# Kernel tuning notes

Hardware: AMD Instinct MI355X
Metric: run time of the kernel (lower is better)

Reference implementation:

```python
import math
import jax, jax.numpy as jnp
import numpy as np

# dims (match init_kwargs)
N, K = 10000, 32            # nodes, padded neighbors per node
IN_F, H, HEADS = 128, 128, 8
T_F, R_F, OUT, LAYERS = 64, 32, 64, 2
HD = H // HEADS
START_T, END_T = 0.25, 0.75
ATTN_NORM = math.sqrt(1.0 / HD)
T_NORM = math.sqrt(1.0 / (T_F // 2))
EPS = 1e-5


def layernorm(x, g, b):
    m = jnp.mean(x, axis=-1, keepdims=True)
    v = jnp.var(x, axis=-1, keepdims=True)
    return (x - m) * jax.lax.rsqrt(v + EPS) * g + b


def t2v(dt, Wt, bt):
    # TimeKernel: linear(1->T_F/2) then interleaved [sin, cos] * norm
    h = dt[..., None] * Wt + bt                      # [..., T_F/2]
    return jnp.stack([jnp.sin(h), jnp.cos(h)], axis=-1).reshape(*h.shape[:-1], T_F) * T_NORM


def tgat_layer(x, neighbors, times, rels, mask,
               Wkqv, Wt, bt, Wtime, Wedge, g1, b1n, g2, b2n, W1, bl1, W2, bl2):
    xn = layernorm(x, g1, b1n)
    kqv = xn @ Wkqv                                  # [N, 3H], chunk order (k, q, v)
    k_, q_, v_ = jnp.split(kqv, 3, axis=1)
    kn = k_[neighbors]                               # [N, K, H] irregular gather
    vn = v_[neighbors]
    # per-node time reference: max over [start_t; masked times] (times>=start_t so start_t covered)
    tmax = jnp.max(jnp.where(mask, times, START_T), axis=1)        # [N]
    tq_emb = t2v(tmax - START_T, Wt, bt)             # [N, T_F] (the prepended start_t row)
    tn_emb = t2v(tmax[:, None] - times, Wt, bt)      # [N, K, T_F]
    t_qq = (tq_emb @ Wtime)[:, H:2 * H]              # query chunk of time KQV
    tkn = tn_emb @ Wtime                             # [N, K, 3H]
    re = rels @ Wedge                                # [N, K, 3H]
    q = q_ + t_qq                                    # [N, H]
    k = kn + tkn[..., :H] + re[..., :H]
    v = vn + tkn[..., 2 * H:] + re[..., 2 * H:]
    qh = q.reshape(N, HEADS, HD)
    kh = k.reshape(N, K, HEADS, HD)
    vh = v.reshape(N, K, HEADS, HD)
    scores = jnp.einsum('nhd,nkhd->nhk', qh, kh) * ATTN_NORM
    scores = jnp.where(mask[:, None, :], scores, -1e30)
    attn = jax.nn.softmax(scores, axis=-1)
    out = jnp.einsum('nhk,nkhd->nhd', attn, vh).reshape(N, H)
    has = jnp.any(mask, axis=1)                      # nodes with zero valid neighbors -> zeros
    h = jnp.where(has[:, None], out, 0.0)
    h2 = h + xn
    hn = layernorm(h2, g2, b2n)
    z = jnp.concatenate([xn, hn], axis=1)
    z = jax.nn.relu(z @ W1 + bl1) @ W2 + bl2
    return z + h2


def setup_inputs() -> dict:
    key = jax.random.key(0)
    ks = jax.random.split(key, 16)
    w = lambda i, *shape: jax.random.normal(ks[i], shape, dtype=jnp.float32) * 0.05
    return {
        'x': jax.random.normal(ks[0], (N, IN_F), dtype=jnp.float32),
        'neighbors': jax.random.randint(ks[1], (N, K), 0, N, dtype=jnp.int32),
        'times': jax.random.uniform(ks[2], (N, K), dtype=jnp.float32),
        'rels': jax.random.normal(ks[3], (N, K, R_F), dtype=jnp.float32),
        'Wp': w(4, IN_F, H), 'bp': jnp.zeros((H,), jnp.float32),
        'Wkqv': w(5, H, 3 * H),
        'Wt': w(6, T_F // 2), 'bt': jnp.zeros((T_F // 2,), jnp.float32),
        'Wtime': w(7, T_F, 3 * H),
        'Wedge': w(8, R_F, 3 * H),
        'g1': jnp.ones((H,), jnp.float32), 'b1n': jnp.zeros((H,), jnp.float32),
        'g2': jnp.ones((H,), jnp.float32), 'b2n': jnp.zeros((H,), jnp.float32),
        'W1': w(9, 2 * H, H), 'bl1': jnp.zeros((H,), jnp.float32),
        'W2': w(10, H, H), 'bl2': jnp.zeros((H,), jnp.float32),
        'Wo': w(11, H, OUT), 'bo': jnp.zeros((OUT,), jnp.float32),
    }


def reference(x, neighbors, times, rels, Wp, bp, Wkqv, Wt, bt, Wtime, Wedge,
              g1, b1n, g2, b2n, W1, bl1, W2, bl2, Wo, bo):
    mask = (times >= START_T) & (times < END_T)      # [N, K] temporal neighbor mask
    h = jax.nn.relu(x @ Wp + bp)
    for _ in range(LAYERS):                          # layers SHARE weights (ModuleList([layer]*layers))
        h = tgat_layer(h, neighbors, times, rels, mask,
                       Wkqv, Wt, bt, Wtime, Wedge, g1, b1n, g2, b2n, W1, bl1, W2, bl2)
    return h @ Wo + bo
```

## Files before the change

### kernel.cpp

```cpp
#include <hip/hip_runtime.h>
#include <hip/hip_bf16.h>

#define NN 10000
#define KK 32
#define HH 128
#define TFH 32
#define RFE 32
#define OUTF 64
#define START_T 0.25f
#define END_T 0.75f
#define ATTN_NORM 0.25f
#define T_NORM 0.17677669529663687f
#define LN_EPS 1e-5f
#define MT 64

typedef __attribute__((ext_vector_type(4))) float f32x4;
typedef __attribute__((ext_vector_type(8))) short bf16x8;

__device__ __forceinline__ ushort f2bf(float x){
  __hip_bfloat16 b = __float2bfloat16(x);
  return *(ushort*)&b;
}
__device__ __forceinline__ float bf2f(ushort u){
  __hip_bfloat16 b = *(__hip_bfloat16*)&u;
  return __bfloat162float(b);
}

__device__ __forceinline__ float groupsum32(float v){
  v += __shfl_xor(v, 16, 32);
  v += __shfl_xor(v, 8, 32);
  v += __shfl_xor(v, 4, 32);
  v += __shfl_xor(v, 2, 32);
  v += __shfl_xor(v, 1, 32);
  return v;
}

__device__ __forceinline__ float wavesum64(float v){
  v += __shfl_xor(v, 32, 64);
  v += __shfl_xor(v, 16, 64);
  v += __shfl_xor(v, 8, 64);
  v += __shfl_xor(v, 4, 64);
  v += __shfl_xor(v, 2, 64);
  v += __shfl_xor(v, 1, 64);
  return v;
}

__global__ __launch_bounds__(256) void k_prep_wT(const float* __restrict__ Wp, const float* __restrict__ Wkqv,
    const float* __restrict__ W1, const float* __restrict__ W2, const float* __restrict__ Wo,
    const float* __restrict__ Wtime, const float* __restrict__ Wedge,
    ushort* __restrict__ WpT, ushort* __restrict__ WkqvT, ushort* __restrict__ W1T,
    ushort* __restrict__ W2T, ushort* __restrict__ WoT, ushort* __restrict__ WcT){
  int id = blockIdx.x*256 + threadIdx.x;
  if (id < 16384){ int n=id>>7, k=id&127; WpT[id]=f2bf(Wp[k*HH+n]); return; }
  id -= 16384;
  if (id < 49152){ int n=id>>7, k=id&127; WkqvT[id]=f2bf(Wkqv[k*384+n]); return; }
  id -= 49152;
  if (id < 32768){ int n=id>>8, k=id&255; W1T[id]=f2bf(W1[k*HH+n]); return; }
  id -= 32768;
  if (id < 16384){ int n=id>>7, k=id&127; W2T[id]=f2bf(W2[k*HH+n]); return; }
  id -= 16384;
  if (id < 8192){ int n=id>>7, k=id&127; WoT[id]=f2bf(Wo[k*OUTF+n]); return; }
  id -= 8192;
  if (id < 24576){
    const int c = id/96, r = id%96;
    const int cc = (c < 128) ? c : (c + 128);
    const float v = (r < 64) ? Wtime[r*384 + cc] : Wedge[(r-64)*384 + cc];
    WcT[c*96 + r] = f2bf(v);
  }
}

#define LDA1 136
#define LDA 104
#define LDKV 264

__global__ __launch_bounds__(256) void k_node_proj(
    const float* __restrict__ X, const ushort* __restrict__ WpT, const float* __restrict__ bp,
    float* __restrict__ Y,
    const float* __restrict__ times, const int* __restrict__ nbrs,
    const float* __restrict__ Wt, const float* __restrict__ bt, const float* __restrict__ Wtime,
    float* __restrict__ tqq, float* __restrict__ tmaxb,
    int* __restrict__ cntb, uint* __restrict__ vmaskb, int* __restrict__ nbrC){
  __shared__ ushort As[16*LDA1];
  __shared__ float temb2[2][2*TFH];
  __shared__ float tmax_sh[2];
  const int tid = threadIdx.x;
  if (blockIdx.x < NN/16){
    const int n0 = blockIdx.x*16;
    #pragma unroll
    for (int p=0;p<2;++p){
      const int idx = tid + p*256;
      const int row = idx>>5, c4 = (idx&31)*4;
      const float4 v = *(const float4*)&X[(size_t)(n0+row)*HH + c4];
      *(ushort4*)&As[row*LDA1 + c4] = make_ushort4(f2bf(v.x), f2bf(v.y), f2bf(v.z), f2bf(v.w));
    }
    __syncthreads();
    const int w = tid>>6, lane = tid&63;
    const int lr = lane&15, lk8 = (lane>>4)*8, rbase = (lane>>4)*4;
    bf16x8 a[4];
    #pragma unroll
    for (int kk=0;kk<4;kk++) a[kk] = *(const bf16x8*)&As[lr*LDA1 + kk*32 + lk8];
    f32x4 acc[2];
    #pragma unroll
    for (int nt=0;nt<2;nt++) acc[nt] = (f32x4){0.f,0.f,0.f,0.f};
    #pragma unroll
    for (int nt=0;nt<2;nt++){
      const int n = w*2 + nt;
      #pragma unroll
      for (int kk=0;kk<4;kk++){
        bf16x8 b = *(const bf16x8*)&WpT[(n*16+lr)*HH + kk*32 + lk8];
        acc[nt] = __builtin_amdgcn_mfma_f32_16x16x32_bf16(a[kk], b, acc[nt],0,0,0);
      }
    }
    #pragma unroll
    for (int nt=0;nt<2;nt++){
      const int c = (w*2+nt)*16 + lr;
      const float bj = bp[c];
      #pragma unroll
      for (int r=0;r<4;r++)
        Y[(size_t)(n0 + rbase + r)*HH + c] = fmaxf(acc[nt][r] + bj, 0.f);
    }
  } else {
    const int node0 = (blockIdx.x - NN/16)*2;
    if (tid < MT){
      const int i = tid>>5, k = tid&31;
      const int node = node0 + i;
      const float t = times[node*KK + k];
      const bool valid = (t >= START_T) && (t < END_T);
      float val = valid ? t : START_T;
      #pragma unroll
      for (int off=16; off; off>>=1) val = fmaxf(val, __shfl_xor(val, off, 32));
      const unsigned long long bal = __ballot(valid);
      const uint vm = (uint)(bal >> (i*32));
      if (valid){
        const int slot = __popc(vm & ((1u<<k)-1));
        nbrC[node*KK + slot] = nbrs[node*KK + k];
      }
      if (k==0){ cntb[node] = __popc(vm); vmaskb[node] = vm; tmaxb[node] = val; tmax_sh[i] = val; }
    }
    __syncthreads();
    if (tid < MT){
      const int i = tid>>5, f = tid&31;
      const float hh = fmaf(tmax_sh[i] - START_T, Wt[f], bt[f]);
      temb2[i][2*f]   = __sinf(hh)*T_NORM;
      temb2[i][2*f+1] = __cosf(hh)*T_NORM;
    }
    __syncthreads();
    {
      const int i = tid>>7, jj = tid&127;
      float acc = 0.f;
      #pragma unroll
      for (int f=0; f<2*TFH; f++) acc = fmaf(temb2[i][f], Wtime[f*384 + HH + jj], acc);
      tqq[(size_t)(node0+i)*HH + jj] = acc;
    }
  }
}

__global__ __launch_bounds__(256) void k_kv0_ln0(
    const float* __restrict__ times, const float* __restrict__ rels, const float* __restrict__ tmaxb,
    const float* __restrict__ Wt, const float* __restrict__ bt, const ushort* __restrict__ WcT,
    const uint* __restrict__ vmaskb, uint4* __restrict__ kvout,
    const float* __restrict__ Hin, const ushort* __restrict__ WkqvT,
    const float* __restrict__ g1, const float* __restrict__ b1, const float* __restrict__ tqq,
    float* __restrict__ XN, ushort* __restrict__ xnb,
    float* __restrict__ Qf, ushort* __restrict__ KVb){
  __shared__ ushort smem[MT*LDKV];
  __shared__ float dt_sh[MT];
  const int tid = threadIdx.x;
  if (blockIdx.x < NN/16){
    ushort* As = smem;
    const int n0 = blockIdx.x*16;
    const int grp = tid>>5, gl = tid&31;
    {
      const float4 gv = *(const float4*)&g1[gl*4];
      const float4 bv = *(const float4*)&b1[gl*4];
      #pragma unroll
      for (int rr=0; rr<2; ++rr){
        const int row = grp + rr*8;
        const int node = n0 + row;
        float4 hv = *(const float4*)&Hin[(size_t)node*HH + gl*4];
        float s = hv.x+hv.y+hv.z+hv.w;
        s = groupsum32(s);
        const float mean = s*(1.f/HH);
        const float dx=hv.x-mean, dy=hv.y-mean, dz=hv.z-mean, dw=hv.w-mean;
        float vs = dx*dx+dy*dy+dz*dz+dw*dw;
        vs = groupsum32(vs);
        const float rstd = rsqrtf(vs*(1.f/HH)+LN_EPS);
        const float x0=dx*rstd*gv.x+bv.x, x1=dy*rstd*gv.y+bv.y, x2=dz*rstd*gv.z+bv.z, x3=dw*rstd*gv.w+bv.w;
        ushort4 pk = make_ushort4(f2bf(x0), f2bf(x1), f2bf(x2), f2bf(x3));
        *(ushort4*)&As[row*LDA1 + gl*4] = pk;
        *(float4*)&XN[(size_t)node*HH + gl*4] = make_float4(x0,x1,x2,x3);
        *(ushort4*)&xnb[(size_t)node*HH + gl*4] = pk;
      }
    }
    __syncthreads();
    const int w = tid>>6, lane = tid&63;
    const int lr = lane&15, lk8 = (lane>>4)*8, rbase = (lane>>4)*4;
    bf16x8 a[4];
    #pragma unroll
    for (int kk=0;kk<4;kk++) a[kk] = *(const bf16x8*)&As[lr*LDA1 + kk*32 + lk8];
    f32x4 acc[6];
    #pragma unroll
    for (int nt=0;nt<6;nt++) acc[nt] = (f32x4){0.f,0.f,0.f,0.f};
    #pragma unroll
    for (int nt=0;nt<6;nt++){
      const int n = w*6 + nt;
      #pragma unroll
      for (int kk=0;kk<4;kk++){
        bf16x8 b = *(const bf16x8*)&WkqvT[(n*16+lr)*HH + kk*32 + lk8];
        acc[nt] = __builtin_amdgcn_mfma_f32_16x16x32_bf16(a[kk], b, acc[nt],0,0,0);
      }
    }
    #pragma unroll
    for (int nt=0;nt<6;nt++){
      const int c = (w*6+nt)*16 + lr;
      #pragma unroll
      for (int r=0;r<4;r++){
        const int node = n0 + rbase + r;
        const float v = acc[nt][r];
        if (c < HH)           KVb[(size_t)node*256 + 2*c] = f2bf(v);
        else if (c < 2*HH)    Qf[(size_t)node*HH + (c-HH)] = v + tqq[(size_t)node*HH + (c-HH)];
        else                  KVb[(size_t)node*256 + 2*(c-2*HH) + 1] = f2bf(v);
      }
    }
  } else {
    ushort* Fa = smem;
    ushort* kvs = smem;
    const int node0 = (blockIdx.x - NN/16)*2;
    if (tid < MT){
      const int node = node0 + (tid>>5);
      dt_sh[tid] = tmaxb[node] - times[node*KK + (tid&31)];
    }
    __syncthreads();
    #pragma unroll
    for (int s0=0; s0<8; ++s0){
      const int s = tid + s0*256;
      const int p = s>>5, f = s&31;
      const float hh = fmaf(dt_sh[p], Wt[f], bt[f]);
      ushort2 pk;
      pk.x = f2bf(__sinf(hh)*T_NORM);
      pk.y = f2bf(__cosf(hh)*T_NORM);
      *(ushort2*)&Fa[p*LDA + 2*f] = pk;
    }
    #pragma unroll
    for (int s0=0; s0<2; ++s0){
      const int i = tid + s0*256;
      const int p = i>>3, seg = i&7;
      const float4 rv = *(const float4*)&rels[((size_t)node0*KK + p)*RFE + seg*4];
      ushort4 w2; w2.x=f2bf(rv.x); w2.y=f2bf(rv.y); w2.z=f2bf(rv.z); w2.w=f2bf(rv.w);
      *(ushort4*)&Fa[p*LDA + 64 + seg*4] = w2;
    }
    __syncthreads();
    const int wave = tid>>6, lane = tid&63;
    const int lr = lane&15, lk = (lane>>4)*8;
    f32x4 acc[4][4];
    #pragma unroll
    for (int m=0;m<4;m++)
      #pragma unroll
      for (int n=0;n<4;n++) acc[m][n] = (f32x4){0.f,0.f,0.f,0.f};
    #pragma unroll
    for (int kk=0; kk<3; ++kk){
      const int k0 = kk*32;
      bf16x8 a[4], b[4];
      #pragma unroll
      for (int m=0;m<4;m++) a[m] = *(const bf16x8*)&Fa[(m*16 + lr)*LDA + k0 + lk];
      #pragma unroll
      for (int n=0;n<4;n++) b[n] = *(const bf16x8*)&WcT[(wave*64 + n*16 + lr)*96 + k0 + lk];
      #pragma unroll
      for (int m=0;m<4;m++)
        #pragma unroll
        for (int n=0;n<4;n++)
          acc[m][n] = __builtin_amdgcn_mfma_f32_16x16x32_bf16(a[m], b[n], acc[m][n], 0,0,0);
    }
    __syncthreads();
    const int rbase = (lane>>4)*4;
    #pragma unroll
    for (int n=0;n<4;n++){
      const int c = wave*64 + n*16 + lr;
      const int ip = (c < 128) ? (2*c) : (2*(c-128)+1);
      #pragma unroll
      for (int m=0;m<4;m++)
        #pragma unroll
        for (int r=0;r<4;r++)
          kvs[(m*16 + rbase + r)*LDKV + ip] = f2bf(acc[m][n][r]);
    }
    __syncthreads();
    const uint vm0 = vmaskb[node0], vm1 = vmaskb[node0+1];
    #pragma unroll
    for (int pass=0; pass<8; ++pass){
      const int idx = pass*256 + tid;
      const int row = idx>>5, seg = idx&31;
      const int nloc = row>>5, k = row&31;
      const uint vm = nloc ? vm1 : vm0;
      if ((vm>>k)&1u){
        const int slot = __popc(vm & ((1u<<k)-1));
        const uint4 v = *(const uint4*)&kvs[row*LDKV + seg*8];
        kvout[((size_t)(node0+nloc)*KK + slot)*32 + seg] = v;
      }
    }
  }
}

__global__ __launch_bounds__(256) void k_ln_kqv_mfma(const float* __restrict__ Hin, const ushort* __restrict__ WkqvT,
    const float* __restrict__ g1, const float* __restrict__ b1, const float* __restrict__ tqq,
    float* __restrict__ XN, ushort* __restrict__ xnb,
    float* __restrict__ Qf, ushort* __restrict__ KVb){
  __shared__ ushort As[16*LDA1];
  const int tid = threadIdx.x, n0 = blockIdx.x*16;
  const int grp = tid>>5, gl = tid&31;
  {
    const float4 gv = *(const float4*)&g1[gl*4];
    const float4 bv = *(const float4*)&b1[gl*4];
    #pragma unroll
    for (int rr=0; rr<2; ++rr){
      const int row = grp + rr*8;
      const int node = n0 + row;
      float4 hv = *(const float4*)&Hin[(size_t)node*HH + gl*4];
      float s = hv.x+hv.y+hv.z+hv.w;
      s = groupsum32(s);
      const float mean = s*(1.f/HH);
      const float dx=hv.x-mean, dy=hv.y-mean, dz=hv.z-mean, dw=hv.w-mean;
      float vs = dx*dx+dy*dy+dz*dz+dw*dw;
      vs = groupsum32(vs);
      const float rstd = rsqrtf(vs*(1.f/HH)+LN_EPS);
      const float x0=dx*rstd*gv.x+bv.x, x1=dy*rstd*gv.y+bv.y, x2=dz*rstd*gv.z+bv.z, x3=dw*rstd*gv.w+bv.w;
      ushort4 pk = make_ushort4(f2bf(x0), f2bf(x1), f2bf(x2), f2bf(x3));
      *(ushort4*)&As[row*LDA1 + gl*4] = pk;
      *(float4*)&XN[(size_t)node*HH + gl*4] = make_float4(x0,x1,x2,x3);
      *(ushort4*)&xnb[(size_t)node*HH + gl*4] = pk;
    }
  }
  __syncthreads();
  const int w = tid>>6, lane = tid&63;
  const int lr = lane&15, lk8 = (lane>>4)*8, rbase = (lane>>4)*4;
  bf16x8 a[4];
  #pragma unroll
  for (int kk=0;kk<4;kk++) a[kk] = *(const bf16x8*)&As[lr*LDA1 + kk*32 + lk8];
  f32x4 acc[6];
  #pragma unroll
  for (int nt=0;nt<6;nt++) acc[nt] = (f32x4){0.f,0.f,0.f,0.f};
  #pragma unroll
  for (int nt=0;nt<6;nt++){
    const int n = w*6 + nt;
    #pragma unroll
    for (int kk=0;kk<4;kk++){
      bf16x8 b = *(const bf16x8*)&WkqvT[(n*16+lr)*HH + kk*32 + lk8];
      acc[nt] = __builtin_amdgcn_mfma_f32_16x16x32_bf16(a[kk], b, acc[nt],0,0,0);
    }
  }
  #pragma unroll
  for (int nt=0;nt<6;nt++){
    const int c = (w*6+nt)*16 + lr;
    #pragma unroll
    for (int r=0;r<4;r++){
      const int node = n0 + rbase + r;
      const float v = acc[nt][r];
      if (c < HH)           KVb[(size_t)node*256 + 2*c] = f2bf(v);
      else if (c < 2*HH)    Qf[(size_t)node*HH + (c-HH)] = v + tqq[(size_t)node*HH + (c-HH)];
      else                  KVb[(size_t)node*256 + 2*(c-2*HH) + 1] = f2bf(v);
    }
  }
}

__global__ __launch_bounds__(256) void k_attn6(
    const float* __restrict__ Qf, const uint2* __restrict__ KVu2, const uint2* __restrict__ kvaddC2,
    const int* __restrict__ nbrC, const int* __restrict__ cntb,
    const float* __restrict__ XN, const float* __restrict__ g2, const float* __restrict__ b2,
    float* __restrict__ H2, ushort* __restrict__ hnb){
  __shared__ int nbr_sh[4][KK];
  const int tid = threadIdx.x, node0 = blockIdx.x*4;
  if (tid < 128) nbr_sh[tid>>5][tid&31] = nbrC[(node0 + (tid>>5))*KK + (tid&31)];
  __syncthreads();
  const int wv = tid>>6, l = tid&63;
  const int node = node0 + wv;
  const int cnt = cntb[node];
  const float2 q2 = *(const float2*)&Qf[(size_t)node*HH + 2*l];
  const float q0s = q2.x * ATTN_NORM, q1s = q2.y * ATTN_NORM;
  const uint2* karow = kvaddC2 + (size_t)node*KK*64 + l;
  float m_ = -3.0e38f, sume = 0.f, a0 = 0.f, a1 = 0.f;
  const int cc = (cnt + 7) >> 3;
  for (int ch=0; ch<cc; ++ch){
    const int base = ch*8;
    uint2 ka[8], kb[8];
    #pragma unroll
    for (int i=0;i<8;i++){
      int slot = base + i; slot = (slot < cnt) ? slot : (cnt-1);
      ka[i] = karow[(size_t)slot*64];
      kb[i] = KVu2[(size_t)nbr_sh[wv][slot]*64 + l];
    }
    float s[8];
    #pragma unroll
    for (int i=0;i<8;i++){
      float p = q0s * (bf2f((ushort)(kb[i].x&0xffff)) + bf2f((ushort)(ka[i].x&0xffff)))
              + q1s * (bf2f((ushort)(kb[i].y&0xffff)) + bf2f((ushort)(ka[i].y&0xffff)));
      p += __shfl_xor(p, 4, 8);
      p += __shfl_xor(p, 2, 8);
      p += __shfl_xor(p, 1, 8);
      s[i] = (base + i < cnt) ? p : -1e30f;
    }
    float cm = s[0];
    #pragma unroll
    for (int i=1;i<8;i++) cm = fmaxf(cm, s[i]);
    const float mn = fmaxf(m_, cm);
    const float sc = __expf(m_ - mn);
    sume *= sc; a0 *= sc; a1 *= sc;
    #pragma unroll
    for (int i=0;i<8;i++){
      const float e = __expf(s[i] - mn);
      sume += e;
      a0 = fmaf(e, bf2f((ushort)(kb[i].x>>16)) + bf2f((ushort)(ka[i].x>>16)), a0);
      a1 = fmaf(e, bf2f((ushort)(kb[i].y>>16)) + bf2f((ushort)(ka[i].y>>16)), a1);
    }
    m_ = mn;
  }
  const float inv = (cnt > 0) ? (1.f / sume) : 0.f;
  const float2 xn2 = *(const float2*)&XN[(size_t)node*HH + 2*l];
  const float h0 = a0*inv + xn2.x;
  const float h1 = a1*inv + xn2.y;
  *(float2*)&H2[(size_t)node*HH + 2*l] = make_float2(h0, h1);
  const float mean = wavesum64(h0 + h1) * (1.f/HH);
  const float d0 = h0 - mean, d1 = h1 - mean;
  const float var = wavesum64(d0*d0 + d1*d1) * (1.f/HH);
  const float rstd = rsqrtf(var + LN_EPS);
  const float2 gv = *(const float2*)&g2[2*l];
  const float2 bv = *(const float2*)&b2[2*l];
  ushort2 hn;
  hn.x = f2bf(d0*rstd*gv.x + bv.x);
  hn.y = f2bf(d1*rstd*gv.y + bv.y);
  *(ushort2*)&hnb[(size_t)node*HH + 2*l] = hn;
}

#define LDA2 264
template<int LAST>
__global__ __launch_bounds__(256) void k_ffn_mfma(const ushort* __restrict__ xnb, const ushort* __restrict__ hnb,
    const float* __restrict__ H2, const ushort* __restrict__ W1T, const float* __restrict__ bl1,
    const ushort* __restrict__ W2T, const float* __restrict__ bl2, float* __restrict__ HOUT,
    const ushort* __restrict__ WoT, const float* __restrict__ bo, float* __restrict__ OUT){
  __shared__ ushort As[16*LDA2];
  __shared__ ushort Ms[16*LDA1];
  const int tid = threadIdx.x, n0 = blockIdx.x*16;
  {
    const int row = tid>>4, c8 = (tid&15)*8;
    *(uint4*)&As[row*LDA2 + c8]       = *(const uint4*)&xnb[(size_t)(n0+row)*HH + c8];
    *(uint4*)&As[row*LDA2 + 128 + c8] = *(const uint4*)&hnb[(size_t)(n0+row)*HH + c8];
  }
  __syncthreads();
  const int w = tid>>6, lane = tid&63;
  const int lr = lane&15, lk8 = (lane>>4)*8, rbase = (lane>>4)*4;
  {
    bf16x8 a[8];
    #pragma unroll
    for (int kk=0;kk<8;kk++) a[kk] = *(const bf16x8*)&As[lr*LDA2 + kk*32 + lk8];
    f32x4 acc[2];
    #pragma unroll
    for (int nt=0;nt<2;nt++) acc[nt] = (f32x4){0.f,0.f,0.f,0.f};
    #pragma unroll
    for (int nt=0;nt<2;nt++){
      const int n = w*2 + nt;
      #pragma unroll
      for (int kk=0;kk<8;kk++){
        bf16x8 b = *(const bf16x8*)&W1T[(n*16+lr)*256 + kk*32 + lk8];
        acc[nt] = __builtin_amdgcn_mfma_f32_16x16x32_bf16(a[kk], b, acc[nt],0,0,0);
      }
    }
    #pragma unroll
    for (int nt=0;nt<2;nt++){
      const int c = (w*2+nt)*16 + lr;
      const float bj = bl1[c];
      #pragma unroll
      for (int r=0;r<4;r++)
        Ms[(rbase+r)*LDA1 + c] = f2bf(fmaxf(acc[nt][r] + bj, 0.f));
    }
  }
  __syncthreads();
  {
    bf16x8 a[4];
    #pragma unroll
    for (int kk=0;kk<4;kk++) a[kk] = *(const bf16x8*)&Ms[lr*LDA1 + kk*32 + lk8];
    f32x4 acc[2];
    #pragma unroll
    for (int nt=0;nt<2;nt++) acc[nt] = (f32x4){0.f,0.f,0.f,0.f};
    #pragma unroll
    for (int nt=0;nt<2;nt++){
      const int n = w*2 + nt;
      #pragma unroll
      for (int kk=0;kk<4;kk++){
        bf16x8 b = *(const bf16x8*)&W2T[(n*16+lr)*HH + kk*32 + lk8];
        acc[nt] = __builtin_amdgcn_mfma_f32_16x16x32_bf16(a[kk], b, acc[nt],0,0,0);
      }
    }
    #pragma unroll
    for (int nt=0;nt<2;nt++){
      const int c = (w*2+nt)*16 + lr;
      const float bj = bl2[c];
      #pragma unroll
      for (int r=0;r<4;r++){
        const size_t node = n0 + rbase + r;
        const float hout = acc[nt][r] + bj + H2[node*HH + c];
        if (LAST){
          ((ushort*)As)[(rbase+r)*LDA1 + c] = f2bf(hout);
        } else {
          HOUT[node*HH + c] = hout;
        }
      }
    }
  }
  if (LAST){
    __syncthreads();
    bf16x8 a[4];
    #pragma unroll
    for (int kk=0;kk<4;kk++) a[kk] = *(const bf16x8*)&((ushort*)As)[lr*LDA1 + kk*32 + lk8];
    f32x4 acc = (f32x4){0.f,0.f,0.f,0.f};
    #pragma unroll
    for (int kk=0;kk<4;kk++){
      bf16x8 b = *(const bf16x8*)&WoT[(w*16+lr)*HH + kk*32 + lk8];
      acc = __builtin_amdgcn_mfma_f32_16x16x32_bf16(a[kk], b, acc,0,0,0);
    }
    const int c = w*16 + lr;
    const float bj = bo[c];
    #pragma unroll
    for (int r=0;r<4;r++)
      OUT[(size_t)(n0 + rbase + r)*OUTF + c] = acc[r] + bj;
  }
}

extern "C" void kernel_launch(void* const* d_in, const int* in_sizes, int n_in,
                              void* d_out, int out_size, void* d_ws, size_t ws_size,
                              hipStream_t stream){
  const float* x         = (const float*)d_in[0];
  const int*   neighbors = (const int*)  d_in[1];
  const float* times     = (const float*)d_in[2];
  const float* rels      = (const float*)d_in[3];
  const float* Wp        = (const float*)d_in[4];
  const float* bp        = (const float*)d_in[5];
  const float* Wkqv      = (const float*)d_in[6];
  const float* Wt        = (const float*)d_in[7];
  const float* bt        = (const float*)d_in[8];
  const float* Wtime     = (const float*)d_in[9];
  const float* Wedge     = (const float*)d_in[10];
  const float* g1        = (const float*)d_in[11];
  const float* b1n       = (const float*)d_in[12];
  const float* g2        = (const float*)d_in[13];
  const float* b2n       = (const float*)d_in[14];
  const float* W1        = (const float*)d_in[15];
  const float* bl1       = (const float*)d_in[16];
  const float* W2        = (const float*)d_in[17];
  const float* bl2       = (const float*)d_in[18];
  const float* Wo        = (const float*)d_in[19];
  const float* bo        = (const float*)d_in[20];
  float* out = (float*)d_out;

  char* ws = (char*)d_ws;
  size_t off = 0;
  auto carve = [&](size_t bytes)->char*{
    char* p = ws + off; off = (off + bytes + 255) & ~(size_t)255; return p;
  };
  float* hA    = (float*)carve((size_t)NN*HH*4);
  float* hB    = (float*)carve((size_t)NN*HH*4);
  float* xn    = (float*)carve((size_t)NN*HH*4);
  float* h2    = (float*)carve((size_t)NN*HH*4);
  float* tqq   = (float*)carve((size_t)NN*HH*4);
  float* Qfp   = (float*)carve((size_t)NN*HH*4);
  float* tmaxb = (float*)carve((size_t)NN*4);
  int*   cntb  = (int*)carve((size_t)NN*4);
  uint*  vmaskb= (uint*)carve((size_t)NN*4);
  int*   nbrC  = (int*)carve((size_t)(NN+4)*KK*4);
  ushort* KVb  = (ushort*)carve((size_t)NN*256*2);
  ushort* xnb  = (ushort*)carve((size_t)NN*HH*2);
  ushort* hnb  = (ushort*)carve((size_t)NN*HH*2);
  ushort* WcTg = (ushort*)carve((size_t)256*96*2);
  ushort* WpT  = (ushort*)carve((size_t)16384*2);
  ushort* WkqvT= (ushort*)carve((size_t)49152*2);
  ushort* W1T  = (ushort*)carve((size_t)32768*2);
  ushort* W2T  = (ushort*)carve((size_t)16384*2);
  ushort* WoT  = (ushort*)carve((size_t)8192*2);
  uint*   kvaddC = (uint*)carve((size_t)NN*KK*256*2);
  (void)ws_size;

  k_prep_wT<<<576, 256, 0, stream>>>(Wp, Wkqv, W1, W2, Wo, Wtime, Wedge,
                                     WpT, WkqvT, W1T, W2T, WoT, WcTg);
  k_node_proj<<<NN/16 + NN/2, 256, 0, stream>>>(x, WpT, bp, hA,
                                                times, neighbors, Wt, bt, Wtime,
                                                tqq, tmaxb, cntb, vmaskb, nbrC);
  k_kv0_ln0<<<NN/16 + NN/2, 256, 0, stream>>>(times, rels, tmaxb, Wt, bt, WcTg, vmaskb,
                                              (uint4*)kvaddC,
                                              hA, WkqvT, g1, b1n, tqq, xn, xnb, Qfp, KVb);
  k_attn6<<<NN/4, 256, 0, stream>>>(Qfp, (const uint2*)KVb, (const uint2*)kvaddC, nbrC, cntb,
                                    xn, g2, b2n, h2, hnb);
  k_ffn_mfma<0><<<NN/16, 256, 0, stream>>>(xnb, hnb, h2, W1T, bl1, W2T, bl2, hB,
                                           WoT, bo, out);
  k_ln_kqv_mfma<<<NN/16, 256, 0, stream>>>(hB, WkqvT, g1, b1n, tqq, xn, xnb, Qfp, KVb);
  k_attn6<<<NN/4, 256, 0, stream>>>(Qfp, (const uint2*)KVb, (const uint2*)kvaddC, nbrC, cntb,
                                    xn, g2, b2n, h2, hnb);
  k_ffn_mfma<1><<<NN/16, 256, 0, stream>>>(xnb, hnb, h2, W1T, bl1, W2T, bl2, hA,
                                           WoT, bo, out);
}
```

Before: 165.5 us.

## Fuse layer-two LayerNorm and KQV projection into the first FFN kernel epilogue

The standalone LayerNorm+KQV kernel is removed. The non-last FFN kernel now keeps its fp32 output tile in shared memory (reusing the As buffer with a float stride) and then does the LayerNorm and the KQV MFMA projection for the same 16 nodes directly. This saves one kernel launch and the global write and re-read of the intermediate hidden buffer, which is also dropped from the workspace. The cost is a larger FFN kernel with more registers and an extra barrier, and in-place reuse of the xnb buffer as both input and output within a block.

```diff
diff --git a/kernel.cpp b/kernel.cpp
--- a/kernel.cpp
+++ b/kernel.cpp
@@ -72,6 +72,7 @@
 #define LDA1 136
 #define LDA 104
 #define LDKV 264
+#define LDH 132
 
 __global__ __launch_bounds__(256) void k_node_proj(
     const float* __restrict__ X, const ushort* __restrict__ WpT, const float* __restrict__ bp,
@@ -296,67 +297,6 @@
         const uint4 v = *(const uint4*)&kvs[row*LDKV + seg*8];
         kvout[((size_t)(node0+nloc)*KK + slot)*32 + seg] = v;
       }
-    }
-  }
-}
-
-__global__ __launch_bounds__(256) void k_ln_kqv_mfma(const float* __restrict__ Hin, const ushort* __restrict__ WkqvT,
-    const float* __restrict__ g1, const float* __restrict__ b1, const float* __restrict__ tqq,
-    float* __restrict__ XN, ushort* __restrict__ xnb,
-    float* __restrict__ Qf, ushort* __restrict__ KVb){
-  __shared__ ushort As[16*LDA1];
-  const int tid = threadIdx.x, n0 = blockIdx.x*16;
-  const int grp = tid>>5, gl = tid&31;
-  {
-    const float4 gv = *(const float4*)&g1[gl*4];
-    const float4 bv = *(const float4*)&b1[gl*4];
-    #pragma unroll
-    for (int rr=0; rr<2; ++rr){
-      const int row = grp + rr*8;
-      const int node = n0 + row;
-      float4 hv = *(const float4*)&Hin[(size_t)node*HH + gl*4];
-      float s = hv.x+hv.y+hv.z+hv.w;
-      s = groupsum32(s);
-      const float mean = s*(1.f/HH);
-      const float dx=hv.x-mean, dy=hv.y-mean, dz=hv.z-mean, dw=hv.w-mean;
-      float vs = dx*dx+dy*dy+dz*dz+dw*dw;
-      vs = groupsum32(vs);
-      const float rstd = rsqrtf(vs*(1.f/HH)+LN_EPS);
-      const float x0=dx*rstd*gv.x+bv.x, x1=dy*rstd*gv.y+bv.y, x2=dz*rstd*gv.z+bv.z, x3=dw*rstd*gv.w+bv.w;
-      ushort4 pk = make_ushort4(f2bf(x0), f2bf(x1), f2bf(x2), f2bf(x3));
-      *(ushort4*)&As[row*LDA1 + gl*4] = pk;
-      *(float4*)&XN[(size_t)node*HH + gl*4] = make_float4(x0,x1,x2,x3);
-      *(ushort4*)&xnb[(size_t)node*HH + gl*4] = pk;
-    }
-  }
-  __syncthreads();
-  const int w = tid>>6, lane = tid&63;
-  const int lr = lane&15, lk8 = (lane>>4)*8, rbase = (lane>>4)*4;
-  bf16x8 a[4];
-  #pragma unroll
-  for (int kk=0;kk<4;kk++) a[kk] = *(const bf16x8*)&As[lr*LDA1 + kk*32 + lk8];
-  f32x4 acc[6];
-  #pragma unroll
-  for (int nt=0;nt<6;nt++) acc[nt] = (f32x4){0.f,0.f,0.f,0.f};
-  #pragma unroll
-  for (int nt=0;nt<6;nt++){
-    const int n = w*6 + nt;
-    #pragma unroll
-    for (int kk=0;kk<4;kk++){
-      bf16x8 b = *(const bf16x8*)&WkqvT[(n*16+lr)*HH + kk*32 + lk8];
-      acc[nt] = __builtin_amdgcn_mfma_f32_16x16x32_bf16(a[kk], b, acc[nt],0,0,0);
-    }
-  }
-  #pragma unroll
-  for (int nt=0;nt<6;nt++){
-    const int c = (w*6+nt)*16 + lr;
-    #pragma unroll
-    for (int r=0;r<4;r++){
-      const int node = n0 + rbase + r;
-      const float v = acc[nt][r];
-      if (c < HH)           KVb[(size_t)node*256 + 2*c] = f2bf(v);
-      else if (c < 2*HH)    Qf[(size_t)node*HH + (c-HH)] = v + tqq[(size_t)node*HH + (c-HH)];
-      else                  KVb[(size_t)node*256 + 2*(c-2*HH) + 1] = f2bf(v);
     }
   }
 }
@@ -433,8 +373,11 @@
 template<int LAST>
 __global__ __launch_bounds__(256) void k_ffn_mfma(const ushort* __restrict__ xnb, const ushort* __restrict__ hnb,
     const float* __restrict__ H2, const ushort* __restrict__ W1T, const float* __restrict__ bl1,
-    const ushort* __restrict__ W2T, const float* __restrict__ bl2, float* __restrict__ HOUT,
-    const ushort* __restrict__ WoT, const float* __restrict__ bo, float* __restrict__ OUT){
+    const ushort* __restrict__ W2T, const float* __restrict__ bl2,
+    const ushort* __restrict__ WoT, const float* __restrict__ bo, float* __restrict__ OUT,
+    const ushort* __restrict__ WkqvT, const float* __restrict__ g1, const float* __restrict__ b1,
+    const float* __restrict__ tqq, float* __restrict__ XN, ushort* __restrict__ xnbO,
+    float* __restrict__ Qf, ushort* __restrict__ KVb){
   __shared__ ushort As[16*LDA2];
   __shared__ ushort Ms[16*LDA1];
   const int tid = threadIdx.x, n0 = blockIdx.x*16;
@@ -499,13 +442,13 @@
         if (LAST){
           ((ushort*)As)[(rbase+r)*LDA1 + c] = f2bf(hout);
         } else {
-          HOUT[node*HH + c] = hout;
+          ((float*)As)[(rbase+r)*LDH + c] = hout;
         }
       }
     }
   }
+  __syncthreads();
   if (LAST){
-    __syncthreads();
     bf16x8 a[4];
     #pragma unroll
     for (int kk=0;kk<4;kk++) a[kk] = *(const bf16x8*)&((ushort*)As)[lr*LDA1 + kk*32 + lk8];
@@ -520,6 +463,59 @@
     #pragma unroll
     for (int r=0;r<4;r++)
       OUT[(size_t)(n0 + rbase + r)*OUTF + c] = acc[r] + bj;
+  } else {
+    const float* Hs = (const float*)As;
+    const int grp = tid>>5, gl = tid&31;
+    {
+      const float4 gv = *(const float4*)&g1[gl*4];
+      const float4 bv = *(const float4*)&b1[gl*4];
+      #pragma unroll
+      for (int rr=0; rr<2; ++rr){
+        const int row = grp + rr*8;
+        const int node = n0 + row;
+        float4 hv = *(const float4*)&Hs[row*LDH + gl*4];
+        float s = hv.x+hv.y+hv.z+hv.w;
+        s = groupsum32(s);
+        const float mean = s*(1.f/HH);
+        const float dx=hv.x-mean, dy=hv.y-mean, dz=hv.z-mean, dw=hv.w-mean;
+        float vs = dx*dx+dy*dy+dz*dz+dw*dw;
+        vs = groupsum32(vs);
+        const float rstd = rsqrtf(vs*(1.f/HH)+LN_EPS);
+        const float x0=dx*rstd*gv.x+bv.x, x1=dy*rstd*gv.y+bv.y, x2=dz*rstd*gv.z+bv.z, x3=dw*rstd*gv.w+bv.w;
+        ushort4 pk = make_ushort4(f2bf(x0), f2bf(x1), f2bf(x2), f2bf(x3));
+        *(ushort4*)&Ms[row*LDA1 + gl*4] = pk;
+        *(float4*)&XN[(size_t)node*HH + gl*4] = make_float4(x0,x1,x2,x3);
+        *(ushort4*)&xnbO[(size_t)node*HH + gl*4] = pk;
+      }
+    }
+    __syncthreads();
+    bf16x8 a[4];
+    #pragma unroll
+    for (int kk=0;kk<4;kk++) a[kk] = *(const bf16x8*)&Ms[lr*LDA1 + kk*32 + lk8];
+    f32x4 acc[6];
+    #pragma unroll
+    for (int nt=0;nt<6;nt++) acc[nt] = (f32x4){0.f,0.f,0.f,0.f};
+    #pragma unroll
+    for (int nt=0;nt<6;nt++){
+      const int n = w*6 + nt;
+      #pragma unroll
+      for (int kk=0;kk<4;kk++){
+        bf16x8 b = *(const bf16x8*)&WkqvT[(n*16+lr)*HH + kk*32 + lk8];
+        acc[nt] = __builtin_amdgcn_mfma_f32_16x16x32_bf16(a[kk], b, acc[nt],0,0,0);
+      }
+    }
+    #pragma unroll
+    for (int nt=0;nt<6;nt++){
+      const int c = (w*6+nt)*16 + lr;
+      #pragma unroll
+      for (int r=0;r<4;r++){
+        const int node = n0 + rbase + r;
+        const float v = acc[nt][r];
+        if (c < HH)           KVb[(size_t)node*256 + 2*c] = f2bf(v);
+        else if (c < 2*HH)    Qf[(size_t)node*HH + (c-HH)] = v + tqq[(size_t)node*HH + (c-HH)];
+        else                  KVb[(size_t)node*256 + 2*(c-2*HH) + 1] = f2bf(v);
+      }
+    }
   }
 }
 
@@ -555,7 +551,6 @@
     char* p = ws + off; off = (off + bytes + 255) & ~(size_t)255; return p;
   };
   float* hA    = (float*)carve((size_t)NN*HH*4);
-  float* hB    = (float*)carve((size_t)NN*HH*4);
   float* xn    = (float*)carve((size_t)NN*HH*4);
   float* h2    = (float*)carve((size_t)NN*HH*4);
   float* tqq   = (float*)carve((size_t)NN*HH*4);
@@ -586,11 +581,12 @@
                                               hA, WkqvT, g1, b1n, tqq, xn, xnb, Qfp, KVb);
   k_attn6<<<NN/4, 256, 0, stream>>>(Qfp, (const uint2*)KVb, (const uint2*)kvaddC, nbrC, cntb,
                                     xn, g2, b2n, h2, hnb);
-  k_ffn_mfma<0><<<NN/16, 256, 0, stream>>>(xnb, hnb, h2, W1T, bl1, W2T, bl2, hB,
-                                           WoT, bo, out);
-  k_ln_kqv_mfma<<<NN/16, 256, 0, stream>>>(hB, WkqvT, g1, b1n, tqq, xn, xnb, Qfp, KVb);
+  k_ffn_mfma<0><<<NN/16, 256, 0, stream>>>(xnb, hnb, h2, W1T, bl1, W2T, bl2,
+                                           WoT, bo, out,
+                                           WkqvT, g1, b1n, tqq, xn, xnb, Qfp, KVb);
   k_attn6<<<NN/4, 256, 0, stream>>>(Qfp, (const uint2*)KVb, (const uint2*)kvaddC, nbrC, cntb,
                                     xn, g2, b2n, h2, hnb);
-  k_ffn_mfma<1><<<NN/16, 256, 0, stream>>>(xnb, hnb, h2, W1T, bl1, W2T, bl2, hA,
-                                           WoT, bo, out);
-}
+  k_ffn_mfma<1><<<NN/16, 256, 0, stream>>>(xnb, hnb, h2, W1T, bl1, W2T, bl2,
+                                           WoT, bo, out,
+                                           WkqvT, g1, b1n, tqq, xn, xnb, Qfp, KVb);
+}
```

New measurement: 161.8 us. 2.3% less time.
